# Kernel optimization log

Measured on AMD Instinct MI355X. Metric: run time of the kernel, lower is better.

The kernel has to match this reference:

```python
import jax, jax.numpy as jnp
import numpy as np

N = 32767      # 2**15 - 1 nodes: complete binary tree, parent(i) = (i-1)//2
IN = 512       # in_channels
H = 256        # hidden_dim
OUT = 1        # output_dim
DEPTH = 15     # number of topological levels (static)


def setup_inputs() -> dict:
    key = jax.random.key(0)
    ks = jax.random.split(key, 8)
    x = jax.random.normal(ks[0], (N, IN), dtype=jnp.float32)
    # complete binary tree edge list: edge_index[0]=child, edge_index[1]=parent
    src = jnp.arange(1, N, dtype=jnp.int32)
    dst = (src - 1) // 2
    edge_index = jnp.stack([src, dst])  # [2, N-1]
    s = 1.0 / np.sqrt(H)  # torch LSTMCell/Linear default uniform init scale
    W_ih = jax.random.uniform(ks[1], (4 * H, IN), minval=-s, maxval=s, dtype=jnp.float32)
    W_hh = jax.random.uniform(ks[2], (4 * H, H), minval=-s, maxval=s, dtype=jnp.float32)
    b_ih = jax.random.uniform(ks[3], (4 * H,), minval=-s, maxval=s, dtype=jnp.float32)
    b_hh = jax.random.uniform(ks[4], (4 * H,), minval=-s, maxval=s, dtype=jnp.float32)
    W_fc = jax.random.uniform(ks[5], (OUT, H), minval=-s, maxval=s, dtype=jnp.float32)
    b_fc = jax.random.uniform(ks[6], (OUT,), minval=-s, maxval=s, dtype=jnp.float32)
    return {"x": x, "edge_index": edge_index, "W_ih": W_ih, "W_hh": W_hh,
            "b_ih": b_ih, "b_hh": b_hh, "W_fc": W_fc, "b_fc": b_fc}


def reference(x, edge_index, W_ih, W_hh, b_ih, b_hh, W_fc, b_fc):
    src, dst = edge_index[0], edge_index[1]
    # children count per parent (matches torch children_count loop)
    cnt = jax.ops.segment_sum(jnp.ones_like(src, dtype=x.dtype), dst, num_segments=N)
    cnt = jnp.maximum(cnt, 1.0)[:, None]  # [N,1]; leaves get zero child state anyway
    h = jnp.zeros((N, H), dtype=x.dtype)
    c = jnp.zeros((N, H), dtype=x.dtype)
    # topological sweep: deepest level first (children processed before parents)
    for d in range(DEPTH - 1, -1, -1):
        lo = 2 ** d - 1
        hi = min(2 ** (d + 1) - 1, N)  # level d node index range (static)
        # mean of already-computed child h/c states, gathered via edge list
        mean_h = jax.ops.segment_sum(h[src], dst, num_segments=N)[lo:hi] / cnt[lo:hi]
        mean_c = jax.ops.segment_sum(c[src], dst, num_segments=N)[lo:hi] / cnt[lo:hi]
        # torch LSTMCell: gates in (i, f, g, o) order
        gates = x[lo:hi] @ W_ih.T + b_ih + mean_h @ W_hh.T + b_hh  # [n_level, 4H]
        i, f, g, o = jnp.split(gates, 4, axis=-1)
        i, f, o = jax.nn.sigmoid(i), jax.nn.sigmoid(f), jax.nn.sigmoid(o)
        g = jnp.tanh(g)
        c_new = f * mean_c + i * g
        h_new = o * jnp.tanh(c_new)
        h = h.at[lo:hi].set(h_new)
        c = c.at[lo:hi].set(c_new)
    pooled = jnp.mean(h, axis=0, keepdims=True)  # [1, H]
    out = pooled @ W_fc.T + b_fc                 # [1, 1]
    return out.squeeze(-1)                       # [1]
```

## Files before the change

kernel.cpp:

```cpp
#include <hip/hip_runtime.h>
#include <math.h>


#define N_NODES 32767
#define N_LEAF0 16383
#define IN_C    512
#define H_C     256

typedef __bf16 bf16x8 __attribute__((ext_vector_type(8)));
typedef __bf16 bf16x4 __attribute__((ext_vector_type(4)));
typedef float  f32x4  __attribute__((ext_vector_type(4)));

__device__ __forceinline__ void gload_lds16(const void* g, void* l) {
    __builtin_amdgcn_global_load_lds(
        (const __attribute__((address_space(1))) unsigned int*)g,
        (__attribute__((address_space(3))) unsigned int*)l,
        16, 0, 0);
}

__device__ __forceinline__ float fast_rcp(float x) { return __builtin_amdgcn_rcpf(x); }
__device__ __forceinline__ float sigm(float x)     { return fast_rcp(1.f + __expf(-x)); }
__device__ __forceinline__ float tanh_fast(float x){ return 2.f * fast_rcp(1.f + __expf(-2.f * x)) - 1.f; }

__global__ __launch_bounds__(256)
void conv_bf16_kernel(const float* __restrict__ src, __bf16* __restrict__ dst,
                      int n8, float scale)
{
    const int i = blockIdx.x * 256 + threadIdx.x;
    if (i < n8) {
        const float4* s4 = (const float4*)src;
        const float4 a = s4[2 * i];
        const float4 b = s4[2 * i + 1];
        bf16x8 o;
        o[0] = (__bf16)(scale * a.x); o[1] = (__bf16)(scale * a.y);
        o[2] = (__bf16)(scale * a.z); o[3] = (__bf16)(scale * a.w);
        o[4] = (__bf16)(scale * b.x); o[5] = (__bf16)(scale * b.y);
        o[6] = (__bf16)(scale * b.z); o[7] = (__bf16)(scale * b.w);
        *(bf16x8*)(dst + 8 * i) = o;
    }
}

__global__ __launch_bounds__(256)
void bulk_xw(const float* __restrict__ x,
             const __bf16* __restrict__ wih,
             const float* __restrict__ b_ih,
             const float* __restrict__ b_hh,
             __bf16* __restrict__ hb,
             float* __restrict__ c,
             __bf16* __restrict__ gx)
{
    __shared__ __bf16 As[128 * 32];
    __shared__ __bf16 Bs[128 * 32];

    const int t    = threadIdx.x;
    const int lane = t & 63;
    const int wv   = t >> 6;
    const int wm   = wv >> 1;
    const int wn   = wv & 1;
    const int quad = lane >> 4;
    const int l15  = lane & 15;
    const int bx   = blockIdx.x;
    const int cb   = bx & 7;
    const int m0   = (bx >> 3) * 128;

    f32x4 acc[4][4];
#pragma unroll
    for (int mi = 0; mi < 4; ++mi)
#pragma unroll
        for (int ni = 0; ni < 4; ++ni) acc[mi][ni] = (f32x4)0.f;

    for (int k0 = 0; k0 < IN_C; k0 += 32) {
#pragma unroll
        for (int e = 0; e < 2; ++e) {
            const int chunk = wv * 2 + e;
            const int nl    = chunk * 16 + (lane >> 2);
            const int q     = (nl >> 4) & 3;
            const int cc    = (nl & 15) + ((nl >> 6) << 4);
            const int grow  = q * H_C + cb * 32 + cc;
            const void* g = (const char*)(wih + grow * IN_C + k0) + (lane & 3) * 16;
            gload_lds16(g, (char*)Bs + chunk * 1024);
        }
        {
            const int row  = t >> 1;
            const int kh   = (t & 1) * 16;
            const int node = min(m0 + row, N_NODES - 1);
            const float4* xs = (const float4*)(x + (size_t)node * IN_C + k0 + kh);
            const float4 v0 = xs[0], v1 = xs[1], v2 = xs[2], v3 = xs[3];
            bf16x8 o0, o1;
            o0[0] = (__bf16)v0.x; o0[1] = (__bf16)v0.y; o0[2] = (__bf16)v0.z; o0[3] = (__bf16)v0.w;
            o0[4] = (__bf16)v1.x; o0[5] = (__bf16)v1.y; o0[6] = (__bf16)v1.z; o0[7] = (__bf16)v1.w;
            o1[0] = (__bf16)v2.x; o1[1] = (__bf16)v2.y; o1[2] = (__bf16)v2.z; o1[3] = (__bf16)v2.w;
            o1[4] = (__bf16)v3.x; o1[5] = (__bf16)v3.y; o1[6] = (__bf16)v3.z; o1[7] = (__bf16)v3.w;
            bf16x8* dst = (bf16x8*)(As + row * 32 + kh);
            dst[0] = o0;
            dst[1] = o1;
        }
        __syncthreads();
        bf16x8 af[4], bfr[4];
#pragma unroll
        for (int mi = 0; mi < 4; ++mi)
            af[mi] = *(const bf16x8*)(As + (wm * 64 + mi * 16 + l15) * 32 + quad * 8);
#pragma unroll
        for (int ni = 0; ni < 4; ++ni)
            bfr[ni] = *(const bf16x8*)(Bs + (wn * 64 + ni * 16 + l15) * 32 + quad * 8);
#pragma unroll
        for (int mi = 0; mi < 4; ++mi)
#pragma unroll
            for (int ni = 0; ni < 4; ++ni)
                acc[mi][ni] = __builtin_amdgcn_mfma_f32_16x16x32_bf16(
                    af[mi], bfr[ni], acc[mi][ni], 0, 0, 0);
        __syncthreads();
    }

    const int CH = cb * 32 + wn * 16 + l15;
    float bs[4];
#pragma unroll
    for (int q = 0; q < 4; ++q) bs[q] = b_ih[q * H_C + CH] + b_hh[q * H_C + CH];

#pragma unroll
    for (int mi = 0; mi < 4; ++mi) {
#pragma unroll
        for (int r = 0; r < 4; ++r) {
            const int m = m0 + wm * 64 + mi * 16 + quad * 4 + r;
            if (m >= N_NODES) continue;
            if (m >= N_LEAF0) {
                const float gi = sigm(acc[mi][0][r] + bs[0]);
                const float gg = tanh_fast(acc[mi][2][r] + bs[2]);
                const float go = sigm(acc[mi][3][r] + bs[3]);
                const float cn = gi * gg;
                const float hn = go * tanh_fast(cn);
                c[(size_t)m * H_C + CH] = cn;
                hb[(size_t)m * H_C + CH] = (__bf16)hn;
            } else {
                bf16x4 g4;
#pragma unroll
                for (int q = 0; q < 4; ++q) g4[q] = (__bf16)acc[mi][q][r];
                *(bf16x4*)(gx + (size_t)m * 1024 + CH * 4) = g4;
            }
        }
    }
}

__global__ __launch_bounds__(256)
void level_hw(const __bf16* __restrict__ whh2,
              const float* __restrict__ b_ih,
              const float* __restrict__ b_hh,
              const __bf16* __restrict__ gx,
              __bf16* __restrict__ hb,
              float* __restrict__ c,
              int lo, int n)
{
    __shared__ __bf16 Bfull[8 * 128 * 32];

    const int t    = threadIdx.x;
    const int lane = t & 63;
    const int wv   = t >> 6;
    const int wm   = wv >> 1;
    const int wn   = wv & 1;
    const int quad = lane >> 4;
    const int l15  = lane & 15;
    const int bx   = blockIdx.x;
    const int cb   = bx & 7;
    const int m0   = (bx >> 3) * 128;

#pragma unroll
    for (int kc = 0; kc < 8; ++kc) {
#pragma unroll
        for (int e = 0; e < 2; ++e) {
            const int chunk = wv * 2 + e;
            const int nl    = chunk * 16 + (lane >> 2);
            const int q     = (nl >> 4) & 3;
            const int cc    = (nl & 15) + ((nl >> 6) << 4);
            const int grow  = q * H_C + cb * 32 + cc;
            const void* g = (const char*)(whh2 + grow * H_C + kc * 32) + (lane & 3) * 16;
            gload_lds16(g, (char*)Bfull + kc * 8192 + chunk * 1024);
        }
    }
    __syncthreads();

    f32x4 acc[4][4];
#pragma unroll
    for (int mi = 0; mi < 4; ++mi)
#pragma unroll
        for (int ni = 0; ni < 4; ++ni) acc[mi][ni] = (f32x4)0.f;

    size_t abase[4];
#pragma unroll
    for (int mi = 0; mi < 4; ++mi) {
        const int node = lo + m0 + wm * 64 + mi * 16 + l15;
        abase[mi] = (size_t)(2 * node + 1) * H_C;
    }

#pragma unroll
    for (int kc = 0; kc < 16; ++kc) {
        bf16x8 af[4], bfr[4];
#pragma unroll
        for (int mi = 0; mi < 4; ++mi)
            af[mi] = *(const bf16x8*)(hb + abase[mi] + kc * 32 + quad * 8);
#pragma unroll
        for (int ni = 0; ni < 4; ++ni)
            bfr[ni] = *(const bf16x8*)(Bfull + (kc & 7) * 4096 +
                                       (wn * 64 + ni * 16 + l15) * 32 + quad * 8);
#pragma unroll
        for (int mi = 0; mi < 4; ++mi)
#pragma unroll
            for (int ni = 0; ni < 4; ++ni)
                acc[mi][ni] = __builtin_amdgcn_mfma_f32_16x16x32_bf16(
                    af[mi], bfr[ni], acc[mi][ni], 0, 0, 0);
    }

    const int CH = cb * 32 + wn * 16 + l15;
    const float bs0 = b_ih[0 * H_C + CH] + b_hh[0 * H_C + CH];
    const float bs1 = b_ih[1 * H_C + CH] + b_hh[1 * H_C + CH];
    const float bs2 = b_ih[2 * H_C + CH] + b_hh[2 * H_C + CH];
    const float bs3 = b_ih[3 * H_C + CH] + b_hh[3 * H_C + CH];

#pragma unroll
    for (int mi = 0; mi < 4; ++mi) {
#pragma unroll
        for (int r = 0; r < 4; ++r) {
            const int m = m0 + wm * 64 + mi * 16 + quad * 4 + r;
            if (m < n) {
                const int node = lo + m;
                const bf16x4 g4 = *(const bf16x4*)(gx + (size_t)node * 1024 + CH * 4);
                const float gi = sigm(acc[mi][0][r] + (float)g4[0] + bs0);
                const float gf = sigm(acc[mi][1][r] + (float)g4[1] + bs1);
                const float gt = tanh_fast(acc[mi][2][r] + (float)g4[2] + bs2);
                const float go = sigm(acc[mi][3][r] + (float)g4[3] + bs3);
                const float mc = 0.5f * (c[(size_t)(2 * node + 1) * H_C + CH] +
                                         c[(size_t)(2 * node + 2) * H_C + CH]);
                const float cn = gf * mc + gi * gt;
                const float hn = go * tanh_fast(cn);
                c[(size_t)node * H_C + CH] = cn;
                hb[(size_t)node * H_C + CH] = (__bf16)hn;
            }
        }
    }
}

__global__ __launch_bounds__(256)
void reduce_rows(const __bf16* __restrict__ hb, float* __restrict__ part)
{
    const int tcol = threadIdx.x;
    const int b = blockIdx.x;
    float s = 0.f;
    for (int r = 0; r < 128; ++r) {
        const int row = b * 128 + r;
        if (row < N_NODES) s += (float)hb[(size_t)row * H_C + tcol];
    }
    part[b * H_C + tcol] = s;
}

__global__ __launch_bounds__(256)
void reduce_final(const float* __restrict__ part,
                  const float* __restrict__ W_fc,
                  const float* __restrict__ b_fc,
                  float* __restrict__ out)
{
    __shared__ float sm[256];
    const int t = threadIdx.x;
    float s = 0.f;
    for (int j = 0; j < 256; ++j) s += part[j * H_C + t];
    s = s * (1.0f / (float)N_NODES) * W_fc[t];
    sm[t] = s;
    __syncthreads();
    for (int st = 128; st > 0; st >>= 1) {
        if (t < st) sm[t] += sm[t + st];
        __syncthreads();
    }
    if (t == 0) out[0] = sm[0] + b_fc[0];
}

extern "C" void kernel_launch(void* const* d_in, const int* in_sizes, int n_in,
                              void* d_out, int out_size, void* d_ws, size_t ws_size,
                              hipStream_t stream)
{
    const float* x    = (const float*)d_in[0];
    const float* W_ih = (const float*)d_in[2];
    const float* W_hh = (const float*)d_in[3];
    const float* b_ih = (const float*)d_in[4];
    const float* b_hh = (const float*)d_in[5];
    const float* W_fc = (const float*)d_in[6];
    const float* b_fc = (const float*)d_in[7];
    float* out = (float*)d_out;

    char* w = (char*)d_ws;
    __bf16* hb   = (__bf16*)w;  w += (size_t)N_NODES * H_C * 2;
    float*  c    = (float*)w;   w += (size_t)N_NODES * H_C * 4;
    __bf16* gx   = (__bf16*)w;  w += (size_t)N_LEAF0 * 1024 * 2;
    __bf16* wihb = (__bf16*)w;  w += (size_t)4 * H_C * IN_C * 2;
    __bf16* whh2 = (__bf16*)w;  w += (size_t)4 * H_C * H_C * 2;
    float*  part = (float*)w;

    {
        const int n8i = (4 * H_C * IN_C) / 8;
        conv_bf16_kernel<<<(n8i + 255) / 256, 256, 0, stream>>>(W_ih, wihb, n8i, 1.0f);
        const int n8h = (4 * H_C * H_C) / 8;
        conv_bf16_kernel<<<(n8h + 255) / 256, 256, 0, stream>>>(W_hh, whh2, n8h, 0.5f);
    }

    bulk_xw<<<2048, 256, 0, stream>>>(x, wihb, b_ih, b_hh, hb, c, gx);

    for (int d = 13; d >= 0; --d) {
        const int n  = 1 << d;
        const int lo = n - 1;
        const int nm = (n + 127) / 128;
        level_hw<<<8 * nm, 256, 0, stream>>>(whh2, b_ih, b_hh, gx, hb, c, lo, n);
    }

    reduce_rows<<<256, 256, 0, stream>>>(hb, part);
    reduce_final<<<1, 256, 0, stream>>>(part, W_fc, b_fc, out);
}
```

Measured before the change: 455.7 us.

## Fuse weight conversion, restructure input GEMM, merge small levels into persistent kernel

Merges the two weight-conversion launches into one kernel. Rewrites the input-projection GEMM so each block keeps a full 64-row bf16 x tile in LDS and streams W_ih directly from global memory. Stores the cell state c in bf16 instead of fp32. Replaces the ten smallest per-level launches with a single persistent 64-block kernel that steps through levels 9..0 using a global atomic barrier. The aim is to cut launch overhead and memory traffic on the latency-bound upper levels, at the cost of lower c precision, reliance on a spin barrier that needs all 64 blocks resident, and no LDS reuse of W_ih.

Measured after the change: 455.8 us. Within noise of the previous version (+0.0%).

```diff
diff --git a/kernel.cpp b/kernel.cpp
--- a/kernel.cpp
+++ b/kernel.cpp
@@ -23,34 +23,127 @@
 __device__ __forceinline__ float tanh_fast(float x){ return 2.f * fast_rcp(1.f + __expf(-2.f * x)) - 1.f; }
 
 __global__ __launch_bounds__(256)
-void conv_bf16_kernel(const float* __restrict__ src, __bf16* __restrict__ dst,
-                      int n8, float scale)
+void conv_weights(const float* __restrict__ wih, const float* __restrict__ whh,
+                  __bf16* __restrict__ wihb, __bf16* __restrict__ whh2)
 {
     const int i = blockIdx.x * 256 + threadIdx.x;
-    if (i < n8) {
-        const float4* s4 = (const float4*)src;
-        const float4 a = s4[2 * i];
-        const float4 b = s4[2 * i + 1];
-        bf16x8 o;
-        o[0] = (__bf16)(scale * a.x); o[1] = (__bf16)(scale * a.y);
-        o[2] = (__bf16)(scale * a.z); o[3] = (__bf16)(scale * a.w);
-        o[4] = (__bf16)(scale * b.x); o[5] = (__bf16)(scale * b.y);
-        o[6] = (__bf16)(scale * b.z); o[7] = (__bf16)(scale * b.w);
-        *(bf16x8*)(dst + 8 * i) = o;
-    }
-}
-
-__global__ __launch_bounds__(256)
+    const float* src; __bf16* dst; float scale; int j;
+    if (i < 65536) { src = wih; dst = wihb; scale = 1.0f; j = i; }
+    else           { src = whh; dst = whh2; scale = 0.5f; j = i - 65536; }
+    const float4* s4 = (const float4*)src;
+    const float4 a = s4[2 * j];
+    const float4 b = s4[2 * j + 1];
+    bf16x8 o;
+    o[0] = (__bf16)(scale * a.x); o[1] = (__bf16)(scale * a.y);
+    o[2] = (__bf16)(scale * a.z); o[3] = (__bf16)(scale * a.w);
+    o[4] = (__bf16)(scale * b.x); o[5] = (__bf16)(scale * b.y);
+    o[6] = (__bf16)(scale * b.z); o[7] = (__bf16)(scale * b.w);
+    *(bf16x8*)(dst + 8 * j) = o;
+}
+
+__global__ __launch_bounds__(256, 2)
 void bulk_xw(const float* __restrict__ x,
-             const __bf16* __restrict__ wih,
+             const __bf16* __restrict__ wihb,
              const float* __restrict__ b_ih,
              const float* __restrict__ b_hh,
              __bf16* __restrict__ hb,
-             float* __restrict__ c,
+             __bf16* __restrict__ cb_,
              __bf16* __restrict__ gx)
 {
-    __shared__ __bf16 As[128 * 32];
-    __shared__ __bf16 Bs[128 * 32];
+    __shared__ __bf16 As[16 * 64 * 32];
+
+    const int t    = threadIdx.x;
+    const int lane = t & 63;
+    const int wv   = t >> 6;
+    const int quad = lane >> 4;
+    const int l15  = lane & 15;
+    const int m0   = blockIdx.x * 64;
+
+    {
+        const int r  = t >> 2;
+        const int ks = (t & 3) * 128;
+        const int node = min(m0 + r, N_NODES - 1);
+        const float* xr = x + (size_t)node * IN_C + ks;
+#pragma unroll
+        for (int j = 0; j < 16; ++j) {
+            const int k = ks + j * 8;
+            const float4 a = *(const float4*)(xr + j * 8);
+            const float4 b = *(const float4*)(xr + j * 8 + 4);
+            bf16x8 o;
+            o[0] = (__bf16)a.x; o[1] = (__bf16)a.y; o[2] = (__bf16)a.z; o[3] = (__bf16)a.w;
+            o[4] = (__bf16)b.x; o[5] = (__bf16)b.y; o[6] = (__bf16)b.z; o[7] = (__bf16)b.w;
+            *(bf16x8*)(As + (k >> 5) * 2048 + r * 32 + (k & 31)) = o;
+        }
+    }
+    __syncthreads();
+
+    for (int sp = 0; sp < 4; ++sp) {
+        const int s  = sp * 4 + wv;
+        const int CH = s * 16 + l15;
+        float bs[4];
+#pragma unroll
+        for (int q = 0; q < 4; ++q) bs[q] = b_ih[q * H_C + CH] + b_hh[q * H_C + CH];
+
+        f32x4 acc[4][4];
+#pragma unroll
+        for (int mi = 0; mi < 4; ++mi)
+#pragma unroll
+            for (int ni = 0; ni < 4; ++ni) acc[mi][ni] = (f32x4)0.f;
+
+#pragma unroll 4
+        for (int kc = 0; kc < 16; ++kc) {
+            bf16x8 af[4], bfr[4];
+#pragma unroll
+            for (int mi = 0; mi < 4; ++mi)
+                af[mi] = *(const bf16x8*)(As + kc * 2048 + (mi * 16 + l15) * 32 + quad * 8);
+#pragma unroll
+            for (int ni = 0; ni < 4; ++ni) {
+                const int grow = ni * 256 + s * 16 + l15;
+                bfr[ni] = *(const bf16x8*)(wihb + (size_t)grow * IN_C + kc * 32 + quad * 8);
+            }
+#pragma unroll
+            for (int mi = 0; mi < 4; ++mi)
+#pragma unroll
+                for (int ni = 0; ni < 4; ++ni)
+                    acc[mi][ni] = __builtin_amdgcn_mfma_f32_16x16x32_bf16(
+                        af[mi], bfr[ni], acc[mi][ni], 0, 0, 0);
+        }
+
+#pragma unroll
+        for (int mi = 0; mi < 4; ++mi) {
+#pragma unroll
+            for (int r = 0; r < 4; ++r) {
+                const int m = m0 + mi * 16 + quad * 4 + r;
+                if (m >= N_NODES) continue;
+                if (m >= N_LEAF0) {
+                    const float gi = sigm(acc[mi][0][r] + bs[0]);
+                    const float gg = tanh_fast(acc[mi][2][r] + bs[2]);
+                    const float go = sigm(acc[mi][3][r] + bs[3]);
+                    const float cn = gi * gg;
+                    const float hn = go * tanh_fast(cn);
+                    cb_[(size_t)m * H_C + CH] = (__bf16)cn;
+                    hb[(size_t)m * H_C + CH] = (__bf16)hn;
+                } else {
+                    bf16x4 g4;
+#pragma unroll
+                    for (int q = 0; q < 4; ++q) g4[q] = (__bf16)acc[mi][q][r];
+                    *(bf16x4*)(gx + (size_t)m * 1024 + CH * 4) = g4;
+                }
+            }
+        }
+    }
+}
+
+__global__ __launch_bounds__(256)
+void level_hw(const __bf16* __restrict__ whh2,
+              const float* __restrict__ b_ih,
+              const float* __restrict__ b_hh,
+              const __bf16* __restrict__ gx,
+              __bf16* __restrict__ hb,
+              __bf16* __restrict__ cb_,
+              int lo, int n)
+{
+    __shared__ __bf16 Bfull[8 * 128 * 32];
 
     const int t    = threadIdx.x;
     const int lane = t & 63;
@@ -63,106 +156,6 @@
     const int cb   = bx & 7;
     const int m0   = (bx >> 3) * 128;
 
-    f32x4 acc[4][4];
-#pragma unroll
-    for (int mi = 0; mi < 4; ++mi)
-#pragma unroll
-        for (int ni = 0; ni < 4; ++ni) acc[mi][ni] = (f32x4)0.f;
-
-    for (int k0 = 0; k0 < IN_C; k0 += 32) {
-#pragma unroll
-        for (int e = 0; e < 2; ++e) {
-            const int chunk = wv * 2 + e;
-            const int nl    = chunk * 16 + (lane >> 2);
-            const int q     = (nl >> 4) & 3;
-            const int cc    = (nl & 15) + ((nl >> 6) << 4);
-            const int grow  = q * H_C + cb * 32 + cc;
-            const void* g = (const char*)(wih + grow * IN_C + k0) + (lane & 3) * 16;
-            gload_lds16(g, (char*)Bs + chunk * 1024);
-        }
-        {
-            const int row  = t >> 1;
-            const int kh   = (t & 1) * 16;
-            const int node = min(m0 + row, N_NODES - 1);
-            const float4* xs = (const float4*)(x + (size_t)node * IN_C + k0 + kh);
-            const float4 v0 = xs[0], v1 = xs[1], v2 = xs[2], v3 = xs[3];
-            bf16x8 o0, o1;
-            o0[0] = (__bf16)v0.x; o0[1] = (__bf16)v0.y; o0[2] = (__bf16)v0.z; o0[3] = (__bf16)v0.w;
-            o0[4] = (__bf16)v1.x; o0[5] = (__bf16)v1.y; o0[6] = (__bf16)v1.z; o0[7] = (__bf16)v1.w;
-            o1[0] = (__bf16)v2.x; o1[1] = (__bf16)v2.y; o1[2] = (__bf16)v2.z; o1[3] = (__bf16)v2.w;
-            o1[4] = (__bf16)v3.x; o1[5] = (__bf16)v3.y; o1[6] = (__bf16)v3.z; o1[7] = (__bf16)v3.w;
-            bf16x8* dst = (bf16x8*)(As + row * 32 + kh);
-            dst[0] = o0;
-            dst[1] = o1;
-        }
-        __syncthreads();
-        bf16x8 af[4], bfr[4];
-#pragma unroll
-        for (int mi = 0; mi < 4; ++mi)
-            af[mi] = *(const bf16x8*)(As + (wm * 64 + mi * 16 + l15) * 32 + quad * 8);
-#pragma unroll
-        for (int ni = 0; ni < 4; ++ni)
-            bfr[ni] = *(const bf16x8*)(Bs + (wn * 64 + ni * 16 + l15) * 32 + quad * 8);
-#pragma unroll
-        for (int mi = 0; mi < 4; ++mi)
-#pragma unroll
-            for (int ni = 0; ni < 4; ++ni)
-                acc[mi][ni] = __builtin_amdgcn_mfma_f32_16x16x32_bf16(
-                    af[mi], bfr[ni], acc[mi][ni], 0, 0, 0);
-        __syncthreads();
-    }
-
-    const int CH = cb * 32 + wn * 16 + l15;
-    float bs[4];
-#pragma unroll
-    for (int q = 0; q < 4; ++q) bs[q] = b_ih[q * H_C + CH] + b_hh[q * H_C + CH];
-
-#pragma unroll
-    for (int mi = 0; mi < 4; ++mi) {
-#pragma unroll
-        for (int r = 0; r < 4; ++r) {
-            const int m = m0 + wm * 64 + mi * 16 + quad * 4 + r;
-            if (m >= N_NODES) continue;
-            if (m >= N_LEAF0) {
-                const float gi = sigm(acc[mi][0][r] + bs[0]);
-                const float gg = tanh_fast(acc[mi][2][r] + bs[2]);
-                const float go = sigm(acc[mi][3][r] + bs[3]);
-                const float cn = gi * gg;
-                const float hn = go * tanh_fast(cn);
-                c[(size_t)m * H_C + CH] = cn;
-                hb[(size_t)m * H_C + CH] = (__bf16)hn;
-            } else {
-                bf16x4 g4;
-#pragma unroll
-                for (int q = 0; q < 4; ++q) g4[q] = (__bf16)acc[mi][q][r];
-                *(bf16x4*)(gx + (size_t)m * 1024 + CH * 4) = g4;
-            }
-        }
-    }
-}
-
-__global__ __launch_bounds__(256)
-void level_hw(const __bf16* __restrict__ whh2,
-              const float* __restrict__ b_ih,
-              const float* __restrict__ b_hh,
-              const __bf16* __restrict__ gx,
-              __bf16* __restrict__ hb,
-              float* __restrict__ c,
-              int lo, int n)
-{
-    __shared__ __bf16 Bfull[8 * 128 * 32];
-
-    const int t    = threadIdx.x;
-    const int lane = t & 63;
-    const int wv   = t >> 6;
-    const int wm   = wv >> 1;
-    const int wn   = wv & 1;
-    const int quad = lane >> 4;
-    const int l15  = lane & 15;
-    const int bx   = blockIdx.x;
-    const int cb   = bx & 7;
-    const int m0   = (bx >> 3) * 128;
-
 #pragma unroll
     for (int kc = 0; kc < 8; ++kc) {
 #pragma unroll
@@ -227,13 +220,119 @@
                 const float gf = sigm(acc[mi][1][r] + (float)g4[1] + bs1);
                 const float gt = tanh_fast(acc[mi][2][r] + (float)g4[2] + bs2);
                 const float go = sigm(acc[mi][3][r] + (float)g4[3] + bs3);
-                const float mc = 0.5f * (c[(size_t)(2 * node + 1) * H_C + CH] +
-                                         c[(size_t)(2 * node + 2) * H_C + CH]);
+                const float mc = 0.5f * ((float)cb_[(size_t)(2 * node + 1) * H_C + CH] +
+                                         (float)cb_[(size_t)(2 * node + 2) * H_C + CH]);
                 const float cn = gf * mc + gi * gt;
                 const float hn = go * tanh_fast(cn);
-                c[(size_t)node * H_C + CH] = cn;
+                cb_[(size_t)node * H_C + CH] = (__bf16)cn;
                 hb[(size_t)node * H_C + CH] = (__bf16)hn;
             }
+        }
+    }
+}
+
+__global__ __launch_bounds__(256)
+void levels_tail(const __bf16* __restrict__ whh2,
+                 const float* __restrict__ b_ih,
+                 const float* __restrict__ b_hh,
+                 const __bf16* __restrict__ gx,
+                 __bf16* __restrict__ hb,
+                 __bf16* __restrict__ cb_,
+                 int* __restrict__ bar)
+{
+    const int t    = threadIdx.x;
+    const int lane = t & 63;
+    const int wv   = t >> 6;
+    const int wm   = wv >> 1;
+    const int wn   = wv & 1;
+    const int quad = lane >> 4;
+    const int l15  = lane & 15;
+    const int b    = blockIdx.x;
+    const int slab = b & 7;
+    const int mg   = b >> 3;
+
+    const int CH = slab * 32 + wn * 16 + l15;
+    const float bs0 = b_ih[0 * H_C + CH] + b_hh[0 * H_C + CH];
+    const float bs1 = b_ih[1 * H_C + CH] + b_hh[1 * H_C + CH];
+    const float bs2 = b_ih[2 * H_C + CH] + b_hh[2 * H_C + CH];
+    const float bs3 = b_ih[3 * H_C + CH] + b_hh[3 * H_C + CH];
+
+    int target = 0;
+
+    for (int d = 9; d >= 0; --d) {
+        const int n  = 1 << d;
+        const int lo = n - 1;
+        if (mg * 64 < n) {
+            const int m0 = mg * 64;
+
+            f32x4 acc[2][4];
+#pragma unroll
+            for (int mi = 0; mi < 2; ++mi)
+#pragma unroll
+                for (int ni = 0; ni < 4; ++ni) acc[mi][ni] = (f32x4)0.f;
+
+            size_t abase[2];
+#pragma unroll
+            for (int mi = 0; mi < 2; ++mi) {
+                const int node = lo + m0 + wm * 32 + mi * 16 + l15;
+                abase[mi] = (size_t)(2 * node + 1) * H_C;
+            }
+
+#pragma unroll 4
+            for (int kc = 0; kc < 16; ++kc) {
+                bf16x8 af[2], bfr[4];
+#pragma unroll
+                for (int mi = 0; mi < 2; ++mi)
+                    af[mi] = *(const bf16x8*)(hb + abase[mi] + kc * 32 + quad * 8);
+#pragma unroll
+                for (int ni = 0; ni < 4; ++ni) {
+                    const int grow = ni * H_C + CH;
+                    bfr[ni] = *(const bf16x8*)(whh2 + (size_t)grow * H_C +
+                                               (kc & 7) * 32 + quad * 8);
+                }
+#pragma unroll
+                for (int mi = 0; mi < 2; ++mi)
+#pragma unroll
+                    for (int ni = 0; ni < 4; ++ni)
+                        acc[mi][ni] = __builtin_amdgcn_mfma_f32_16x16x32_bf16(
+                            af[mi], bfr[ni], acc[mi][ni], 0, 0, 0);
+            }
+
+#pragma unroll
+            for (int mi = 0; mi < 2; ++mi) {
+#pragma unroll
+                for (int r = 0; r < 4; ++r) {
+                    const int m = m0 + wm * 32 + mi * 16 + quad * 4 + r;
+                    if (m < n) {
+                        const int node = lo + m;
+                        const bf16x4 g4 = *(const bf16x4*)(gx + (size_t)node * 1024 + CH * 4);
+                        const float gi = sigm(acc[mi][0][r] + (float)g4[0] + bs0);
+                        const float gf = sigm(acc[mi][1][r] + (float)g4[1] + bs1);
+                        const float gt = tanh_fast(acc[mi][2][r] + (float)g4[2] + bs2);
+                        const float go = sigm(acc[mi][3][r] + (float)g4[3] + bs3);
+                        const float mc = 0.5f * ((float)cb_[(size_t)(2 * node + 1) * H_C + CH] +
+                                                 (float)cb_[(size_t)(2 * node + 2) * H_C + CH]);
+                        const float cn = gf * mc + gi * gt;
+                        const float hn = go * tanh_fast(cn);
+                        cb_[(size_t)node * H_C + CH] = (__bf16)cn;
+                        hb[(size_t)node * H_C + CH] = (__bf16)hn;
+                    }
+                }
+            }
+        }
+
+        if (d > 0) {
+            __syncthreads();
+            target += 64;
+            if (t == 0) {
+                __threadfence();
+                atomicAdd(bar, 1);
+                while (__hip_atomic_load(bar, __ATOMIC_RELAXED,
+                                         __HIP_MEMORY_SCOPE_AGENT) < target)
+                    __builtin_amdgcn_s_sleep(8);
+                __threadfence();
+            }
+            __syncthreads();
         }
     }
 }
@@ -286,27 +385,27 @@
 
     char* w = (char*)d_ws;
     __bf16* hb   = (__bf16*)w;  w += (size_t)N_NODES * H_C * 2;
-    float*  c    = (float*)w;   w += (size_t)N_NODES * H_C * 4;
+    __bf16* cb_  = (__bf16*)w;  w += (size_t)N_NODES * H_C * 2;
     __bf16* gx   = (__bf16*)w;  w += (size_t)N_LEAF0 * 1024 * 2;
     __bf16* wihb = (__bf16*)w;  w += (size_t)4 * H_C * IN_C * 2;
     __bf16* whh2 = (__bf16*)w;  w += (size_t)4 * H_C * H_C * 2;
-    float*  part = (float*)w;
-
-    {
-        const int n8i = (4 * H_C * IN_C) / 8;
-        conv_bf16_kernel<<<(n8i + 255) / 256, 256, 0, stream>>>(W_ih, wihb, n8i, 1.0f);
-        const int n8h = (4 * H_C * H_C) / 8;
-        conv_bf16_kernel<<<(n8h + 255) / 256, 256, 0, stream>>>(W_hh, whh2, n8h, 0.5f);
-    }
-
-    bulk_xw<<<2048, 256, 0, stream>>>(x, wihb, b_ih, b_hh, hb, c, gx);
-
-    for (int d = 13; d >= 0; --d) {
+    float*  part = (float*)w;   w += (size_t)256 * H_C * 4;
+    int*    bar  = (int*)w;
+
+    hipMemsetAsync(bar, 0, sizeof(int), stream);
+
+    conv_weights<<<384, 256, 0, stream>>>(W_ih, W_hh, wihb, whh2);
+
+    bulk_xw<<<512, 256, 0, stream>>>(x, wihb, b_ih, b_hh, hb, cb_, gx);
+
+    for (int d = 13; d >= 10; --d) {
         const int n  = 1 << d;
         const int lo = n - 1;
-        const int nm = (n + 127) / 128;
-        level_hw<<<8 * nm, 256, 0, stream>>>(whh2, b_ih, b_hh, gx, hb, c, lo, n);
-    }
+        const int nm = n / 128;
+        level_hw<<<8 * nm, 256, 0, stream>>>(whh2, b_ih, b_hh, gx, hb, cb_, lo, n);
+    }
+
+    levels_tail<<<64, 256, 0, stream>>>(whh2, b_ih, b_hh, gx, hb, cb_, bar);
 
     reduce_rows<<<256, 256, 0, stream>>>(hb, part);
     reduce_final<<<1, 256, 0, stream>>>(part, W_fc, b_fc, out);
```
